# Kernel optimization log

Hardware: AMD Instinct MI355X
Metric: run time of the kernel (lower is better)

Reference implementation:

```python
import jax, jax.numpy as jnp
import numpy as np

NA = 100000   # authors
NP_ = 100000  # papers
D = 128       # hidden dim
H = 4         # heads
DH = 32       # head dim (D = H*DH)
L = 2         # layers
R = 3         # relations: 0=writes(a->p), 1=rev_writes(p->a), 2=cites(p->p)
E = 400000    # edges per relation
OUT = 40


def setup_inputs() -> dict:
    key = jax.random.key(0)
    ks = jax.random.split(key, 16)
    s = 0.05
    return {
        "x_author": jax.random.normal(ks[0], (NA, D), jnp.float32),
        "x_paper": jax.random.normal(ks[1], (NP_, D), jnp.float32),
        "ei_writes": jax.random.randint(ks[2], (2, E), 0, NA, dtype=jnp.int32),
        "ei_rev": jax.random.randint(ks[3], (2, E), 0, NA, dtype=jnp.int32),
        "ei_cites": jax.random.randint(ks[4], (2, E), 0, NP_, dtype=jnp.int32),
        "proj_w": jax.random.normal(ks[5], (2, D, D), jnp.float32) * s,
        "proj_b": jax.random.normal(ks[6], (2, D), jnp.float32) * s,
        "kqv_w": jax.random.normal(ks[7], (L, 3, 2, D, D), jnp.float32) * s,  # [layer, {k,q,v}, type, D, D]
        "kqv_b": jax.random.normal(ks[8], (L, 3, 2, D), jnp.float32) * s,
        "out_w": jax.random.normal(ks[9], (L, 2, D, D), jnp.float32) * s,
        "out_b": jax.random.normal(ks[10], (L, 2, D), jnp.float32) * s,
        "rel_a": jax.random.normal(ks[11], (L, R, H, DH, DH), jnp.float32) * s,
        "rel_m": jax.random.normal(ks[12], (L, R, H, DH, DH), jnp.float32) * s,
        "p_rel": jnp.ones((L, R, H), jnp.float32),
        "skip": jnp.ones((L, 2), jnp.float32),
        "cls_w": jax.random.normal(ks[13], (D, OUT), jnp.float32) * s,
        "cls_b": jnp.zeros((OUT,), jnp.float32),
    }


def _seg_softmax(sc, dst, n):
    # softmax over incoming edges grouped by destination node; sc: [E,H]
    m = jax.ops.segment_max(sc, dst, num_segments=n)
    m = jnp.where(jnp.isfinite(m), m, 0.0)
    e = jnp.exp(sc - m[dst])
    z = jax.ops.segment_sum(e, dst, num_segments=n)
    return e / (z[dst] + 1e-16)


def _hgt_layer(h_a, h_p, ei_w, ei_r, ei_c, kqv_w, kqv_b, out_w, out_b, rel_a, rel_m, p_rel, skip):
    na, npp = h_a.shape[0], h_p.shape[0]

    def kqv(h, t):
        k = (h @ kqv_w[0, t] + kqv_b[0, t]).reshape(-1, H, DH)
        q = (h @ kqv_w[1, t] + kqv_b[1, t]).reshape(-1, H, DH)
        v = (h @ kqv_w[2, t] + kqv_b[2, t]).reshape(-1, H, DH)
        return k, q, v

    k_a, q_a, v_a = kqv(h_a, 0)
    k_p, q_p, v_p = kqv(h_p, 1)
    scale = 1.0 / jnp.sqrt(jnp.float32(DH))

    def edge_msgs(k_src, v_src, q_dst, ei, r):
        ke = jnp.einsum('ehd,hdf->ehf', k_src[ei[0]], rel_a[r])
        ve = jnp.einsum('ehd,hdf->ehf', v_src[ei[0]], rel_m[r])
        sc = (q_dst[ei[1]] * ke).sum(-1) * p_rel[r] * scale  # [E,H]
        return sc, ve

    # destination = paper: writes (r=0) + cites (r=2); softmax jointly per dst node
    sc_w, ve_w = edge_msgs(k_a, v_a, q_p, ei_w, 0)
    sc_c, ve_c = edge_msgs(k_p, v_p, q_p, ei_c, 2)
    sc_p = jnp.concatenate([sc_w, sc_c], 0)
    ve_p = jnp.concatenate([ve_w, ve_c], 0)
    dst_p = jnp.concatenate([ei_w[1], ei_c[1]], 0)
    al_p = _seg_softmax(sc_p, dst_p, npp)
    agg_p = jax.ops.segment_sum(ve_p * al_p[..., None], dst_p, num_segments=npp).reshape(npp, D)

    # destination = author: rev_writes (r=1)
    sc_r, ve_r = edge_msgs(k_p, v_p, q_a, ei_r, 1)
    al_a = _seg_softmax(sc_r, ei_r[1], na)
    agg_a = jax.ops.segment_sum(ve_r * al_a[..., None], ei_r[1], num_segments=na).reshape(na, D)

    def out_mix(agg, h, t):
        o = jax.nn.gelu(agg, approximate=False) @ out_w[t] + out_b[t]
        s = jax.nn.sigmoid(skip[t])
        return s * o + (1.0 - s) * h

    # HGTNet.forward applies ELU after each HGTConv (dropout is identity in eval mode)
    h_a = jax.nn.elu(out_mix(agg_a, h_a, 0))
    h_p = jax.nn.elu(out_mix(agg_p, h_p, 1))
    return h_a, h_p


def reference(x_author, x_paper, ei_writes, ei_rev, ei_cites, proj_w, proj_b,
              kqv_w, kqv_b, out_w, out_b, rel_a, rel_m, p_rel, skip, cls_w, cls_b):
    h_a = x_author @ proj_w[0] + proj_b[0]
    h_p = x_paper @ proj_w[1] + proj_b[1]
    for l in range(L):
        h_a, h_p = _hgt_layer(h_a, h_p, ei_writes, ei_rev, ei_cites,
                              kqv_w[l], kqv_b[l], out_w[l], out_b[l],
                              rel_a[l], rel_m[l], p_rel[l], skip[l])
    return h_p @ cls_w + cls_b
```

## Files before the change

kernel.cpp:

```cpp
#include <hip/hip_runtime.h>
#include <hip/hip_bf16.h>
#include <math.h>

constexpr int NA  = 100000;
constexpr int NPP = 100000;
constexpr int D   = 128;
constexpr int H   = 4;
constexpr int E   = 400000;
constexpr int R   = 3;
constexpr int L   = 2;
constexpr int NSLOT = 23;
constexpr int SLOT_ELEMS = 8 * 4 * 512;
constexpr int GB2c = (NA + 127) / 128;
constexpr int GAc  = NA / 8;

using s8v = __attribute__((ext_vector_type(8))) short;
using f4v = __attribute__((ext_vector_type(4))) float;
typedef unsigned short ushort_t;

static __device__ __forceinline__ unsigned short f2bf(float f) {
  unsigned u = __float_as_uint(f);
  return (unsigned short)((u + 0x7fffu + ((u >> 16) & 1u)) >> 16);
}
static __device__ __forceinline__ float bf2f(unsigned short s) {
  return __uint_as_float(((unsigned)s) << 16);
}
static __device__ __forceinline__ float klo(int i) {
  return __uint_as_float(((unsigned)i) << 16);
}
static __device__ __forceinline__ float vhi(int i) {
  return __uint_as_float(((unsigned)i) & 0xffff0000u);
}
static __device__ __forceinline__ float gelu_f(float x) {
  return 0.5f * x * (1.0f + erff(x * 0.70710678118654752f));
}
static __device__ __forceinline__ float elu_f(float x) {
  return x > 0.0f ? x : expm1f(x);
}

static __device__ __forceinline__ void load_a2(
    const ushort_t* __restrict__ A, int ar0, int ar1, int ks, int g,
    s8v& a0, s8v& a1) {
  const ushort_t* ap0 = A + (size_t)ar0 * 128 + ks * 32 + g * 4;
  ushort4 u0 = *(const ushort4*)ap0;
  ushort4 u1 = *(const ushort4*)(ap0 + 16);
  a0[0]=(short)u0.x; a0[1]=(short)u0.y; a0[2]=(short)u0.z; a0[3]=(short)u0.w;
  a0[4]=(short)u1.x; a0[5]=(short)u1.y; a0[6]=(short)u1.z; a0[7]=(short)u1.w;
  const ushort_t* ap1 = A + (size_t)ar1 * 128 + ks * 32 + g * 4;
  ushort4 v0 = *(const ushort4*)ap1;
  ushort4 v1 = *(const ushort4*)(ap1 + 16);
  a1[0]=(short)v0.x; a1[1]=(short)v0.y; a1[2]=(short)v0.z; a1[3]=(short)v0.w;
  a1[4]=(short)v1.x; a1[5]=(short)v1.y; a1[6]=(short)v1.z; a1[7]=(short)v1.w;
}

template<bool GELU_A, bool MIX>
__device__ __forceinline__ void dev_gemm8(
    const ushort_t* __restrict__ A, const ushort_t* __restrict__ Bhi,
    const float* __restrict__ bias, ushort_t* __restrict__ Cout,
    const float* __restrict__ skip_ptr, int M, int bx, ushort_t* Bs) {
  for (int i = threadIdx.x; i < 2048; i += 256)
    *(s8v*)&Bs[i * 8] = *(const s8v*)(Bhi + (size_t)i * 8);
  __syncthreads();
  const int lane = threadIdx.x & 63;
  const int wave = threadIdx.x >> 6;
  const int row0 = bx * 128 + wave * 32;
  const int g = lane >> 4, li = lane & 15;
  f4v acc0[8], acc1[8];
#pragma unroll
  for (int ct = 0; ct < 8; ++ct) {
    acc0[ct] = f4v{0.f, 0.f, 0.f, 0.f};
    acc1[ct] = f4v{0.f, 0.f, 0.f, 0.f};
  }
  int ar0 = row0 + li;       if (ar0 >= M) ar0 = M - 1;
  int ar1 = row0 + 16 + li;  if (ar1 >= M) ar1 = M - 1;
#pragma unroll
  for (int ks = 0; ks < 4; ++ks) {
    s8v a0, a1;
    load_a2(A, ar0, ar1, ks, g, a0, a1);
    if (GELU_A) {
#pragma unroll
      for (int i = 0; i < 8; ++i) {
        a0[i] = (short)f2bf(gelu_f(bf2f((unsigned short)a0[i])));
        a1[i] = (short)f2bf(gelu_f(bf2f((unsigned short)a1[i])));
      }
    }
#pragma unroll
    for (int ct = 0; ct < 8; ++ct) {
      s8v bhi = *(const s8v*)&Bs[(ct * 4 + ks) * 512 + lane * 8];
      acc0[ct] = __builtin_amdgcn_mfma_f32_16x16x32_bf16(a0, bhi, acc0[ct], 0, 0, 0);
      acc1[ct] = __builtin_amdgcn_mfma_f32_16x16x32_bf16(a1, bhi, acc1[ct], 0, 0, 0);
    }
  }
  float sskip = 0.f;
  if (MIX) sskip = 1.f / (1.f + __expf(-*skip_ptr));
#pragma unroll
  for (int rf = 0; rf < 2; ++rf) {
#pragma unroll
    for (int ct = 0; ct < 8; ++ct) {
      int col = ct * 16 + li;
      float bv = bias[col];
      f4v a = rf ? acc1[ct] : acc0[ct];
#pragma unroll
      for (int r = 0; r < 4; ++r) {
        int grow = row0 + rf * 16 + g * 4 + r;
        if (grow < M) {
          float v = a[r] + bv;
          size_t off = (size_t)grow * 128 + col;
          if constexpr (MIX) {
            float hprev = bf2f(Cout[off]);
            Cout[off] = f2bf(elu_f(sskip * v + (1.f - sskip) * hprev));
          } else {
            Cout[off] = f2bf(v);
          }
        }
      }
    }
  }
}

__device__ __forceinline__ void dev_gemm_kv(
    const ushort_t* __restrict__ A, const ushort_t* __restrict__ Bkv,
    const float* __restrict__ bias, ushort_t* __restrict__ kvout,
    int M, int bx, int ch, ushort_t* Bs) {
  for (int i = threadIdx.x; i < 2048; i += 256) {
    int kvh = i >> 10, j = i & 1023;
    const ushort_t* src = Bkv + (size_t)kvh * SLOT_ELEMS + ch * 8192 + j * 8;
    *(s8v*)&Bs[kvh * 8192 + j * 8] = *(const s8v*)src;
  }
  __syncthreads();
  const int lane = threadIdx.x & 63;
  const int wave = threadIdx.x >> 6;
  const int row0 = bx * 128 + wave * 32;
  const int g = lane >> 4, li = lane & 15;
  f4v acc0[8], acc1[8];
#pragma unroll
  for (int t = 0; t < 8; ++t) {
    acc0[t] = f4v{0.f, 0.f, 0.f, 0.f};
    acc1[t] = f4v{0.f, 0.f, 0.f, 0.f};
  }
  int ar0 = row0 + li;       if (ar0 >= M) ar0 = M - 1;
  int ar1 = row0 + 16 + li;  if (ar1 >= M) ar1 = M - 1;
#pragma unroll
  for (int ks = 0; ks < 4; ++ks) {
    s8v a0, a1;
    load_a2(A, ar0, ar1, ks, g, a0, a1);
#pragma unroll
    for (int t = 0; t < 4; ++t) {
      s8v kh = *(const s8v*)&Bs[(t * 4 + ks) * 512 + lane * 8];
      acc0[t] = __builtin_amdgcn_mfma_f32_16x16x32_bf16(a0, kh, acc0[t], 0, 0, 0);
      acc1[t] = __builtin_amdgcn_mfma_f32_16x16x32_bf16(a1, kh, acc1[t], 0, 0, 0);
      s8v vh = *(const s8v*)&Bs[8192 + (t * 4 + ks) * 512 + lane * 8];
      acc0[4 + t] = __builtin_amdgcn_mfma_f32_16x16x32_bf16(a0, vh, acc0[4 + t], 0, 0, 0);
      acc1[4 + t] = __builtin_amdgcn_mfma_f32_16x16x32_bf16(a1, vh, acc1[4 + t], 0, 0, 0);
    }
  }
#pragma unroll
  for (int rf = 0; rf < 2; ++rf) {
#pragma unroll
    for (int t = 0; t < 4; ++t) {
      int col = ch * 64 + t * 16 + li;
      float bk = bias[col], bv = bias[128 + col];
#pragma unroll
      for (int r = 0; r < 4; ++r) {
        int grow = row0 + rf * 16 + g * 4 + r;
        if (grow < M) {
          float kvl = rf ? acc1[t][r] : acc0[t][r];
          float vvl = rf ? acc1[4 + t][r] : acc0[4 + t][r];
          ushort2 o;
          o.x = f2bf(kvl + bk);
          o.y = f2bf(vvl + bv);
          *(ushort2*)(kvout + (size_t)grow * 256 + 2 * col) = o;
        }
      }
    }
  }
}

__device__ __forceinline__ void dev_proj(
    const float* __restrict__ A, const ushort_t* __restrict__ Bhi,
    const ushort_t* __restrict__ Blo, const float* __restrict__ bias,
    ushort_t* __restrict__ Cout, int M, int bx, ushort_t* Bs) {
  for (int i = threadIdx.x; i < 4096; i += 256) {
    int half = i >> 11, j = i & 2047;
    const ushort_t* src = (half ? Blo : Bhi) + (size_t)j * 8;
    *(s8v*)&Bs[half * 16384 + j * 8] = *(const s8v*)src;
  }
  __syncthreads();
  const int lane = threadIdx.x & 63;
  const int wave = threadIdx.x >> 6;
  const int row0 = bx * 128 + wave * 32;
  const int g = lane >> 4, li = lane & 15;
  f4v acc0[8], acc1[8];
#pragma unroll
  for (int ct = 0; ct < 8; ++ct) {
    acc0[ct] = f4v{0.f, 0.f, 0.f, 0.f};
    acc1[ct] = f4v{0.f, 0.f, 0.f, 0.f};
  }
  int ar0 = row0 + li;       if (ar0 >= M) ar0 = M - 1;
  int ar1 = row0 + 16 + li;  if (ar1 >= M) ar1 = M - 1;
#pragma unroll
  for (int ks = 0; ks < 4; ++ks) {
    s8v ahi[2];
#pragma unroll
    for (int rf = 0; rf < 2; ++rf) {
      int ar = rf ? ar1 : ar0;
      const float* ap = A + (size_t)ar * 128 + ks * 32 + g * 4;
      float4 u0 = *(const float4*)ap;
      float4 u1 = *(const float4*)(ap + 16);
      float x[8] = {u0.x, u0.y, u0.z, u0.w, u1.x, u1.y, u1.z, u1.w};
#pragma unroll
      for (int i = 0; i < 8; ++i) ahi[rf][i] = (short)f2bf(x[i]);
    }
#pragma unroll
    for (int ct = 0; ct < 8; ++ct) {
      const ushort_t* bp = &Bs[(ct * 4 + ks) * 512 + lane * 8];
      s8v bhi = *(const s8v*)bp;
      s8v blo = *(const s8v*)(bp + 16384);
      acc0[ct] = __builtin_amdgcn_mfma_f32_16x16x32_bf16(ahi[0], bhi, acc0[ct], 0, 0, 0);
      acc1[ct] = __builtin_amdgcn_mfma_f32_16x16x32_bf16(ahi[1], bhi, acc1[ct], 0, 0, 0);
      acc0[ct] = __builtin_amdgcn_mfma_f32_16x16x32_bf16(ahi[0], blo, acc0[ct], 0, 0, 0);
      acc1[ct] = __builtin_amdgcn_mfma_f32_16x16x32_bf16(ahi[1], blo, acc1[ct], 0, 0, 0);
    }
  }
#pragma unroll
  for (int rf = 0; rf < 2; ++rf) {
#pragma unroll
    for (int ct = 0; ct < 8; ++ct) {
      int col = ct * 16 + li;
      float bv = bias[col];
      f4v a = rf ? acc1[ct] : acc0[ct];
#pragma unroll
      for (int r = 0; r < 4; ++r) {
        int grow = row0 + rf * 16 + g * 4 + r;
        if (grow < M) Cout[(size_t)grow * 128 + col] = f2bf(a[r] + bv);
      }
    }
  }
}

template<bool SEL>
__device__ __forceinline__ void dev_attn_m(
    const int* __restrict__ rp, const int* __restrict__ col,
    const ushort_t* __restrict__ kv, const ushort_t* __restrict__ q,
    float prW, float prC, ushort_t* __restrict__ aggout, int ablk) {
  int lane = threadIdx.x & 63;
  int wave = threadIdx.x >> 6;
  int half = lane >> 5;
  int l32  = lane & 31;
  int dst  = ablk * 8 + wave * 2 + half;
  ushort4 qv = *(const ushort4*)(q + (size_t)dst * D + l32 * 4);
  float q0 = bf2f(qv.x), q1 = bf2f(qv.y), q2 = bf2f(qv.z), q3 = bf2f(qv.w);
  int e0 = rp[dst];
  int dt = rp[dst + 1] - e0;
  float z = 0.f, a0 = 0.f, a1 = 0.f, a2 = 0.f, a3 = 0.f;
  for (int jj = 0; jj < dt; jj += 4) {
    int4 us[4]; bool vs[4]; float prs[4];
#pragma unroll
    for (int s2 = 0; s2 < 4; ++s2) {
      int idx = jj + s2;
      bool v = idx < dt;
      int ci = e0 + (v ? idx : 0);
      int row = col[ci];
      us[s2] = *(const int4*)(kv + (size_t)row * 256 + l32 * 8);
      vs[s2] = v;
      prs[s2] = SEL ? ((row >= NA) ? prC : prW) : prW;
    }
#pragma unroll
    for (int s2 = 0; s2 < 4; ++s2) {
      float p = q0 * klo(us[s2].x) + q1 * klo(us[s2].y)
              + q2 * klo(us[s2].z) + q3 * klo(us[s2].w);
      p += __shfl_xor(p, 1);
      p += __shfl_xor(p, 2);
      p += __shfl_xor(p, 4);
      float e = vs[s2] ? __expf(p * prs[s2]) : 0.f;
      z  += e;
      a0 += e * vhi(us[s2].x);
      a1 += e * vhi(us[s2].y);
      a2 += e * vhi(us[s2].z);
      a3 += e * vhi(us[s2].w);
    }
  }
  float inv = 1.f / (z + 1e-16f);
  ushort4 o;
  o.x = f2bf(a0 * inv);
  o.y = f2bf(a1 * inv);
  o.z = f2bf(a2 * inv);
  o.w = f2bf(a3 * inv);
  *(ushort4*)(aggout + (size_t)dst * D + l32 * 4) = o;
}

__device__ __forceinline__ void dev_count(const int* __restrict__ dst,
                                          int* __restrict__ deg, int bidx) {
  for (int e = bidx * 256 + (int)threadIdx.x; e < E; e += 256 * 256)
    atomicAdd(&deg[dst[e]], 1);
}
__device__ __forceinline__ void dev_fill(const int* __restrict__ ei,
                                         const int* __restrict__ rp,
                                         int* __restrict__ cnt,
                                         int* __restrict__ col, int bidx, int off) {
  const int* dst = ei + E;
  for (int e = bidx * 256 + (int)threadIdx.x; e < E; e += 256 * 256) {
    int d = dst[e];
    int pos = atomicAdd(&cnt[d], 1);
    col[rp[d] + pos] = ei[e] + off;
  }
}

__global__ __launch_bounds__(256, 2) void fusedProj(
    const float* __restrict__ x_a, const float* __restrict__ x_p,
    const ushort_t* __restrict__ B0h, const ushort_t* __restrict__ B0l,
    const ushort_t* __restrict__ B1h, const ushort_t* __restrict__ B1l,
    const float* __restrict__ proj_b,
    ushort_t* __restrict__ h_a, ushort_t* __restrict__ h_p,
    const int* __restrict__ ei_w, const int* __restrict__ ei_c,
    const int* __restrict__ ei_r, int* __restrict__ degz) {
  __shared__ ushort_t Bs[32768];
  unsigned b = blockIdx.x;
  if (b % 3 == 2) {
    int ci = b / 3;
    if (ci < 768) {
      int rel = ci >> 8, sub = ci & 255;
      const int* dst = rel == 0 ? ei_w + E : rel == 1 ? ei_c + E : ei_r + E;
      int* deg = (rel == 2) ? (degz + NPP) : degz;
      dev_count(dst, deg, sub);
    }
  } else {
    int gi = b - (b + 1) / 3;
    if (gi < GB2c) dev_proj(x_a, B0h, B0l, proj_b,     h_a, NA,  gi, Bs);
    else           dev_proj(x_p, B1h, B1l, proj_b + D, h_p, NPP, gi - GB2c, Bs);
  }
}

__device__ __forceinline__ void dev_biggemm_slice(
    int slice, int bx,
    const ushort_t* h_a, const ushort_t* h_p,
    const ushort_t* Bqa, const ushort_t* Bqp,
    const ushort_t* BkvR, const ushort_t* BkvW, const ushort_t* BkvC,
    const float* bqa, const float* bqp,
    const float* cbR, const float* cbW, const float* cbC,
    ushort_t* b_q, ushort_t* b_q2,
    ushort_t* kvR, ushort_t* kvP, ushort_t* Bs) {
  if (slice == 0)      dev_gemm8<false, false>(h_a, Bqa, bqa, b_q,  nullptr, NA,  bx, Bs);
  else if (slice == 1) dev_gemm8<false, false>(h_p, Bqp, bqp, b_q2, nullptr, NPP, bx, Bs);
  else if (slice <= 3) dev_gemm_kv(h_p, BkvR, cbR, kvR, NPP, bx, slice - 2, Bs);
  else if (slice <= 5) dev_gemm_kv(h_a, BkvW, cbW, kvP, NA,  bx, slice - 4, Bs);
  else                 dev_gemm_kv(h_p, BkvC, cbC, kvP + (size_t)NA * 256, NPP, bx, slice - 6, Bs);
}

__global__ __launch_bounds__(256, 4) void biggemm(
    const ushort_t* __restrict__ h_a, const ushort_t* __restrict__ h_p,
    const ushort_t* __restrict__ Bqa, const ushort_t* __restrict__ Bqp,
    const ushort_t* __restrict__ BkvR, const ushort_t* __restrict__ BkvW,
    const ushort_t* __restrict__ BkvC,
    const float* __restrict__ bqa, const float* __restrict__ bqp,
    const float* __restrict__ cbR, const float* __restrict__ cbW,
    const float* __restrict__ cbC,
    ushort_t* __restrict__ b_q, ushort_t* __restrict__ b_q2,
    ushort_t* __restrict__ kvR, ushort_t* __restrict__ kvP) {
  __shared__ ushort_t Bs[16384];
  dev_biggemm_slice(blockIdx.y, blockIdx.x, h_a, h_p, Bqa, Bqp, BkvR, BkvW, BkvC,
                    bqa, bqp, cbR, cbW, cbC, b_q, b_q2, kvR, kvP, Bs);
}

__global__ __launch_bounds__(256, 4) void fusedFill(
    const ushort_t* __restrict__ h_a, const ushort_t* __restrict__ h_p,
    const ushort_t* __restrict__ Bqa, const ushort_t* __restrict__ Bqp,
    const ushort_t* __restrict__ BkvR, const ushort_t* __restrict__ BkvW,
    const ushort_t* __restrict__ BkvC,
    const float* __restrict__ bqa, const float* __restrict__ bqp,
    const float* __restrict__ cbR, const float* __restrict__ cbW,
    const float* __restrict__ cbC,
    ushort_t* __restrict__ b_q, ushort_t* __restrict__ b_q2,
    ushort_t* __restrict__ kvR, ushort_t* __restrict__ kvP,
    const int* __restrict__ ei_w, const int* __restrict__ ei_c,
    const int* __restrict__ ei_r,
    const int* __restrict__ rp_p, const int* __restrict__ rp_r,
    int* __restrict__ cntz, int* __restrict__ col_p, int* __restrict__ col_r) {
  __shared__ ushort_t Bs[16384];
  unsigned b = blockIdx.x;
  if (b % 9 == 8) {
    int fi = b / 9;
    if (fi < 768) {
      int rel = fi >> 8, sub = fi & 255;
      if (rel == 0)      dev_fill(ei_w, rp_p, cntz,       col_p, sub, 0);
      else if (rel == 1) dev_fill(ei_c, rp_p, cntz,       col_p, sub, NA);
      else               dev_fill(ei_r, rp_r, cntz + NPP, col_r, sub, 0);
    }
  } else {
    int gi = b - (b + 1) / 9;
    int slice = gi & 7, bx = gi >> 3;
    if (bx < GB2c)
      dev_biggemm_slice(slice, bx, h_a, h_p, Bqa, Bqp, BkvR, BkvW, BkvC,
                        bqa, bqp, cbR, cbW, cbC, b_q, b_q2, kvR, kvP, Bs);
  }
}

__global__ __launch_bounds__(256, 8) void bigattn(
    const int* __restrict__ rp_r, const int* __restrict__ col_r,
    const ushort_t* __restrict__ kvR, ushort_t* __restrict__ q_a,
    const int* __restrict__ rp_p, const int* __restrict__ col_p,
    const ushort_t* __restrict__ kvP, ushort_t* __restrict__ q_p,
    const float* __restrict__ prelR, const float* __restrict__ prelW,
    const float* __restrict__ prelC) {
  unsigned x = blockIdx.x;
  int head = (threadIdx.x & 31) >> 3;
  const float scale = 0.17677669529663688f;
  if (x & 1) {
    float pr = prelR[head] * scale;
    dev_attn_m<false>(rp_r, col_r, kvR, q_a, pr, pr, q_a, (int)(x >> 1));
  } else {
    dev_attn_m<true>(rp_p, col_p, kvP, q_p,
                     prelW[head] * scale, prelC[head] * scale, q_p, (int)(x >> 1));
  }
}

__global__ __launch_bounds__(256, 4) void bigmix(
    const ushort_t* __restrict__ agg_a, const ushort_t* __restrict__ Bo0,
    const float* __restrict__ ob0, ushort_t* __restrict__ h_a,
    const float* __restrict__ sk0,
    const ushort_t* __restrict__ agg_p, const ushort_t* __restrict__ Bo1,
    const float* __restrict__ ob1, ushort_t* __restrict__ h_p,
    const float* __restrict__ sk1) {
  __shared__ ushort_t Bs[16384];
  if (blockIdx.y == 0) dev_gemm8<true, true>(agg_a, Bo0, ob0, h_a, sk0, NA,  blockIdx.x, Bs);
  else                 dev_gemm8<true, true>(agg_p, Bo1, ob1, h_p, sk1, NPP, blockIdx.x, Bs);
}

__global__ __launch_bounds__(256, 4) void gemm_cls(
    const ushort_t* __restrict__ A,
    const ushort_t* __restrict__ Bhi, const ushort_t* __restrict__ Blo,
    const float* __restrict__ bias, float* __restrict__ Cv, int M) {
  constexpr int NT16 = 3;
  constexpr int HN = NT16 * 2048;
  __shared__ ushort_t Bs[HN * 2];
  for (int i = threadIdx.x; i < (HN / 8) * 2; i += 256) {
    int half = i / (HN / 8), j = i % (HN / 8);
    const ushort_t* src = (half ? Blo : Bhi) + (size_t)j * 8;
    *(s8v*)&Bs[half * HN + j * 8] = *(const s8v*)src;
  }
  __syncthreads();
  const int lane = threadIdx.x & 63;
  const int wave = threadIdx.x >> 6;
  const int row0 = blockIdx.x * 128 + wave * 32;
  const int g = lane >> 4, li = lane & 15;
  f4v acc0[NT16], acc1[NT16];
#pragma unroll
  for (int ct = 0; ct < NT16; ++ct) {
    acc0[ct] = f4v{0.f, 0.f, 0.f, 0.f};
    acc1[ct] = f4v{0.f, 0.f, 0.f, 0.f};
  }
  int ar0 = row0 + li;       if (ar0 >= M) ar0 = M - 1;
  int ar1 = row0 + 16 + li;  if (ar1 >= M) ar1 = M - 1;
#pragma unroll
  for (int ks = 0; ks < 4; ++ks) {
    s8v a0, a1;
    load_a2(A, ar0, ar1, ks, g, a0, a1);
#pragma unroll
    for (int ct = 0; ct < NT16; ++ct) {
      const ushort_t* bp = &Bs[(ct * 4 + ks) * 512 + lane * 8];
      s8v bhi = *(const s8v*)bp;
      s8v blo = *(const s8v*)(bp + HN);
      acc0[ct] = __builtin_amdgcn_mfma_f32_16x16x32_bf16(a0, bhi, acc0[ct], 0, 0, 0);
      acc1[ct] = __builtin_amdgcn_mfma_f32_16x16x32_bf16(a1, bhi, acc1[ct], 0, 0, 0);
      acc0[ct] = __builtin_amdgcn_mfma_f32_16x16x32_bf16(a0, blo, acc0[ct], 0, 0, 0);
      acc1[ct] = __builtin_amdgcn_mfma_f32_16x16x32_bf16(a1, blo, acc1[ct], 0, 0, 0);
    }
  }
#pragma unroll
  for (int rf = 0; rf < 2; ++rf) {
#pragma unroll
    for (int ct = 0; ct < NT16; ++ct) {
      int col = ct * 16 + li;
      bool colok = (col < 40);
      float bv = colok ? bias[col] : 0.f;
      f4v a = rf ? acc1[ct] : acc0[ct];
#pragma unroll
      for (int r = 0; r < 4; ++r) {
        int grow = row0 + rf * 16 + g * 4 + r;
        if (grow < M && colok) Cv[(size_t)grow * 40 + col] = a[r] + bv;
      }
    }
  }
}

__global__ __launch_bounds__(256) void combine_w(
    const float* __restrict__ kqv_w, const float* __restrict__ kqv_b,
    const float* __restrict__ rel_a, const float* __restrict__ rel_m,
    float* __restrict__ cw, float* __restrict__ cb) {
  int b  = blockIdx.x;
  int kv = b & 1;
  int r  = (b >> 1) % R;
  int l  = b / (2 * R);
  int t_src = (r == 0) ? 0 : 1;
  int i_w   = (kv == 0) ? 0 : 2;
  const float* W    = kqv_w + ((size_t)((l*3 + i_w)*2 + t_src)) * D * D;
  const float* bvec = kqv_b + ((size_t)((l*3 + i_w)*2 + t_src)) * D;
  const float* rel  = ((kv == 0) ? rel_a : rel_m) + ((size_t)(l*R + r)) * H * 32 * 32;
  float* Cout = cw + (size_t)b * D * D;
  float* cbo  = cb + (size_t)b * D;
  for (int idx = threadIdx.x; idx < D * D; idx += 256) {
    int i = idx / D, j = idx % D;
    int h = j >> 5, f = j & 31;
    const float* relh = rel + h * 32 * 32;
    float sum = 0.f;
#pragma unroll
    for (int d = 0; d < 32; ++d) sum += W[i*D + (h*32 + d)] * relh[d*32 + f];
    Cout[idx] = sum;
  }
  if (threadIdx.x < D) {
    int j = threadIdx.x;
    int h = j >> 5, f = j & 31;
    const float* relh = rel + h * 32 * 32;
    float sum = 0.f;
#pragma unroll
    for (int d = 0; d < 32; ++d) sum += bvec[h*32 + d] * relh[d*32 + f];
    cbo[j] = sum;
  }
}

__global__ __launch_bounds__(256) void pack_b(
    const float* __restrict__ proj_w, const float* __restrict__ kqv_w,
    const float* __restrict__ out_w, const float* __restrict__ cls_w,
    const float* __restrict__ cw,
    ushort_t* __restrict__ phi, ushort_t* __restrict__ plo) {
  int slot = blockIdx.x;
  const float* src; int ncol = 128;
  if (slot == 0) src = proj_w;
  else if (slot == 1) src = proj_w + D * D;
  else if (slot == 22) { src = cls_w; ncol = 40; }
  else {
    int l = (slot - 2) / 10, k = (slot - 2) % 10;
    if (k == 0)      src = kqv_w + ((size_t)((l*3 + 1)*2 + 0)) * D * D;
    else if (k == 1) src = kqv_w + ((size_t)((l*3 + 1)*2 + 1)) * D * D;
    else if (k < 8)  { int idx = k - 2; src = cw + ((size_t)((l*R)*2 + idx)) * D * D; }
    else             src = out_w + ((size_t)(l*2 + (k - 8))) * D * D;
  }
  int nt = (ncol + 15) / 16;
  int total = nt * 4 * 512;
  ushort_t* ph = phi + (size_t)slot * SLOT_ELEMS;
  ushort_t* pl = plo + (size_t)slot * SLOT_ELEMS;
  for (int idx = threadIdx.x; idx < total; idx += 256) {
    int j = idx & 7, lane = (idx >> 3) & 63, ks = (idx >> 9) & 3, ct = idx >> 11;
    int k = 4 * (lane >> 4) + (j & 3) + 16 * (j >> 2) + 32 * ks;
    int n = ct * 16 + (lane & 15);
    float v = (n < ncol) ? src[(size_t)k * ncol + n] : 0.f;
    unsigned short h = f2bf(v);
    ph[idx] = h;
    pl[idx] = f2bf(v - bf2f(h));
  }
}

__global__ __launch_bounds__(256) void scan_partial(const int* __restrict__ degz,
                                                    int* __restrict__ bsum) {
  int blk = blockIdx.x, rel = blk / 25, t25 = blk % 25;
  const int* deg = degz + rel * NPP + t25 * 4096;
  int nrem = min(4096, NPP - t25 * 4096);
  int base = threadIdx.x * 16;
  int s = 0;
  if (base < nrem) {
#pragma unroll
    for (int i4 = 0; i4 < 4; ++i4) {
      int4 v = *(const int4*)(deg + base + i4 * 4);
      s += v.x + v.y + v.z + v.w;
    }
  }
  __shared__ int sm[256];
  sm[threadIdx.x] = s; __syncthreads();
  for (int o = 128; o > 0; o >>= 1) {
    if (threadIdx.x < o) sm[threadIdx.x] += sm[threadIdx.x + o];
    __syncthreads();
  }
  if (threadIdx.x == 0) bsum[blk] = sm[0];
}
__global__ __launch_bounds__(256) void scan_final(const int* __restrict__ degz,
                                                  const int* __restrict__ bsum,
                                                  int* rp_p, int* rp_r) {
  int blk = blockIdx.x, rel = blk / 25, t25 = blk % 25;
  const int* deg = degz + rel * NPP + t25 * 4096;
  int* rpb = (rel == 0 ? rp_p : rp_r);
  int* rp = rpb + t25 * 4096;
  int boffv = 0;
  for (int i = 0; i < t25; ++i) boffv += bsum[rel * 25 + i];
  int nrem = min(4096, NPP - t25 * 4096);
  int base = threadIdx.x * 16;
  bool ok = base < nrem;
  int v[16]; int s = 0;
  if (ok) {
#pragma unroll
    for (int i4 = 0; i4 < 4; ++i4) {
      int4 u = *(const int4*)(deg + base + i4 * 4);
      v[i4*4+0] = u.x; v[i4*4+1] = u.y; v[i4*4+2] = u.z; v[i4*4+3] = u.w;
      s += u.x + u.y + u.z + u.w;
    }
  }
  __shared__ int sm[256];
  sm[threadIdx.x] = s; __syncthreads();
  for (int o = 1; o < 256; o <<= 1) {
    int x = (threadIdx.x >= o) ? sm[threadIdx.x - o] : 0;
    __syncthreads(); sm[threadIdx.x] += x; __syncthreads();
  }
  int run = boffv + sm[threadIdx.x] - s;
  if (ok) {
    int w[16];
#pragma unroll
    for (int i = 0; i < 16; ++i) { w[i] = run; run += v[i]; }
#pragma unroll
    for (int i4 = 0; i4 < 4; ++i4) *(int4*)(rp + base + i4 * 4) = *(const int4*)&w[i4*4];
  }
  if (t25 == 24 && threadIdx.x == 255) rpb[NPP] = boffv + sm[255];
}

extern "C" void kernel_launch(void* const* d_in, const int* in_sizes, int n_in,
                              void* d_out, int out_size, void* d_ws, size_t ws_size,
                              hipStream_t stream) {
  const float* x_a    = (const float*)d_in[0];
  const float* x_p    = (const float*)d_in[1];
  const int*   ei_w   = (const int*)d_in[2];
  const int*   ei_r   = (const int*)d_in[3];
  const int*   ei_c   = (const int*)d_in[4];
  const float* proj_w = (const float*)d_in[5];
  const float* proj_b = (const float*)d_in[6];
  const float* kqv_w  = (const float*)d_in[7];
  const float* kqv_b  = (const float*)d_in[8];
  const float* out_w  = (const float*)d_in[9];
  const float* out_b  = (const float*)d_in[10];
  const float* rel_a  = (const float*)d_in[11];
  const float* rel_m  = (const float*)d_in[12];
  const float* p_rel  = (const float*)d_in[13];
  const float* skip   = (const float*)d_in[14];
  const float* cls_w  = (const float*)d_in[15];
  const float* cls_b  = (const float*)d_in[16];
  float* out = (float*)d_out;

  const size_t NF = (size_t)NA * D;
  char* p = (char*)d_ws;
  float* cw = (float*)p;              p += (size_t)12 * D * D * 4;
  float* cb = (float*)p;              p += (size_t)12 * D * 4;
  ushort_t* h_a   = (ushort_t*)p;     p += NF * 2;
  ushort_t* h_p   = (ushort_t*)p;     p += NF * 2;
  ushort_t* b_q   = (ushort_t*)p;     p += NF * 2;
  ushort_t* b_q2  = (ushort_t*)p;     p += NF * 2;
  ushort_t* b_kvR = (ushort_t*)p;     p += 2 * NF * 2;
  ushort_t* b_kvP = (ushort_t*)p;     p += 4 * NF * 2;
  ushort_t* phi = (ushort_t*)p;       p += (size_t)NSLOT * SLOT_ELEMS * 2;
  ushort_t* plo = (ushort_t*)p;       p += (size_t)NSLOT * SLOT_ELEMS * 2;
  int* rp_p = (int*)p;                p += (NPP + 1) * 4;
  int* rp_r = (int*)p;                p += (NA + 1) * 4;
  int* degz = (int*)p;                p += (size_t)2 * NPP * 4;
  int* cntz = (int*)p;                p += (size_t)2 * NPP * 4;
  int* col_p = (int*)p;               p += (size_t)2 * E * 4;
  int* col_r = (int*)p;               p += (size_t)E * 4;
  int* bsum = (int*)p;                p += 128 * 4;
  if (ws_size < (size_t)(p - (char*)d_ws)) return;

  hipMemsetAsync(degz, 0, sizeof(int) * 4 * (size_t)NPP, stream);

  combine_w<<<12, 256, 0, stream>>>(kqv_w, kqv_b, rel_a, rel_m, cw, cb);
  pack_b<<<NSLOT, 256, 0, stream>>>(proj_w, kqv_w, out_w, cls_w, cw, phi, plo);

  auto PH = [&](int s){ return phi + (size_t)s * SLOT_ELEMS; };
  auto PL = [&](int s){ return plo + (size_t)s * SLOT_ELEMS; };

  fusedProj<<<2346, 256, 0, stream>>>(
      x_a, x_p, PH(0), PL(0), PH(1), PL(1), proj_b, h_a, h_p,
      ei_w, ei_c, ei_r, degz);
  scan_partial<<<50, 256, 0, stream>>>(degz, bsum);
  scan_final<<<50, 256, 0, stream>>>(degz, bsum, rp_p, rp_r);

  for (int l = 0; l < L; ++l) {
    const int SQA = 2 + l * 10 + 0, SQP = 2 + l * 10 + 1;
    auto SKV = [&](int r){ return 2 + l * 10 + 2 + r * 2; };
    const int SO0 = 2 + l * 10 + 8, SO1 = 2 + l * 10 + 9;
    const float* bq_a = kqv_b + ((size_t)((l*3 + 1)*2 + 0)) * D;
    const float* bq_p = kqv_b + ((size_t)((l*3 + 1)*2 + 1)) * D;
    auto CB2 = [&](int r){ return cb + ((size_t)((l*R + r)*2)) * D; };
    const float* prelW = p_rel + (size_t)(l*R + 0) * H;
    const float* prelR = p_rel + (size_t)(l*R + 1) * H;
    const float* prelC = p_rel + (size_t)(l*R + 2) * H;

    if (l == 0) {
      fusedFill<<<7038, 256, 0, stream>>>(
          h_a, h_p, PH(SQA), PH(SQP), PH(SKV(1)), PH(SKV(0)), PH(SKV(2)),
          bq_a, bq_p, CB2(1), CB2(0), CB2(2),
          b_q, b_q2, b_kvR, b_kvP,
          ei_w, ei_c, ei_r, rp_p, rp_r, cntz, col_p, col_r);
    } else {
      biggemm<<<dim3(GB2c, 8), 256, 0, stream>>>(
          h_a, h_p, PH(SQA), PH(SQP), PH(SKV(1)), PH(SKV(0)), PH(SKV(2)),
          bq_a, bq_p, CB2(1), CB2(0), CB2(2),
          b_q, b_q2, b_kvR, b_kvP);
    }
    bigattn<<<2 * GAc, 256, 0, stream>>>(
        rp_r, col_r, b_kvR, b_q,
        rp_p, col_p, b_kvP, b_q2,
        prelR, prelW, prelC);
    bigmix<<<dim3(GB2c, 2), 256, 0, stream>>>(
        b_q,  PH(SO0), out_b + (size_t)(l*2 + 0) * D, h_a, skip + l*2 + 0,
        b_q2, PH(SO1), out_b + (size_t)(l*2 + 1) * D, h_p, skip + l*2 + 1);
  }

  gemm_cls<<<dim3(GB2c, 1), 256, 0, stream>>>(
      h_p, PH(22), PL(22), cls_b, out, NPP);
}
```

Baseline: 781.9 us.

## Drop low-half weight split in input projection and unroll paper attention deeper

The input projection GEMM no longer uses the hi/lo bf16 weight split. It loads only the high half into shared memory, which halves the MFMA count, halves LDS use, and raises launch bounds occupancy from 2 to 4. Separately, the attention gather loop is templated on its unroll factor, and paper-destination nodes (more incoming edges) now issue 8 loads in flight instead of 4. The cost is lower projection precision, since the weights are now single bf16, and higher register pressure in the attention kernel.

```diff
diff --git a/kernel.cpp b/kernel.cpp
--- a/kernel.cpp
+++ b/kernel.cpp
@@ -178,13 +178,10 @@
 
 __device__ __forceinline__ void dev_proj(
     const float* __restrict__ A, const ushort_t* __restrict__ Bhi,
-    const ushort_t* __restrict__ Blo, const float* __restrict__ bias,
-    ushort_t* __restrict__ Cout, int M, int bx, ushort_t* Bs) {
-  for (int i = threadIdx.x; i < 4096; i += 256) {
-    int half = i >> 11, j = i & 2047;
-    const ushort_t* src = (half ? Blo : Bhi) + (size_t)j * 8;
-    *(s8v*)&Bs[half * 16384 + j * 8] = *(const s8v*)src;
-  }
+    const float* __restrict__ bias, ushort_t* __restrict__ Cout,
+    int M, int bx, ushort_t* Bs) {
+  for (int i = threadIdx.x; i < 2048; i += 256)
+    *(s8v*)&Bs[i * 8] = *(const s8v*)(Bhi + (size_t)i * 8);
   __syncthreads();
   const int lane = threadIdx.x & 63;
   const int wave = threadIdx.x >> 6;
@@ -213,13 +210,9 @@
     }
 #pragma unroll
     for (int ct = 0; ct < 8; ++ct) {
-      const ushort_t* bp = &Bs[(ct * 4 + ks) * 512 + lane * 8];
-      s8v bhi = *(const s8v*)bp;
-      s8v blo = *(const s8v*)(bp + 16384);
+      s8v bhi = *(const s8v*)&Bs[(ct * 4 + ks) * 512 + lane * 8];
       acc0[ct] = __builtin_amdgcn_mfma_f32_16x16x32_bf16(ahi[0], bhi, acc0[ct], 0, 0, 0);
       acc1[ct] = __builtin_amdgcn_mfma_f32_16x16x32_bf16(ahi[1], bhi, acc1[ct], 0, 0, 0);
-      acc0[ct] = __builtin_amdgcn_mfma_f32_16x16x32_bf16(ahi[0], blo, acc0[ct], 0, 0, 0);
-      acc1[ct] = __builtin_amdgcn_mfma_f32_16x16x32_bf16(ahi[1], blo, acc1[ct], 0, 0, 0);
     }
   }
 #pragma unroll
@@ -238,7 +231,7 @@
   }
 }
 
-template<bool SEL>
+template<bool SEL, int UN>
 __device__ __forceinline__ void dev_attn_m(
     const int* __restrict__ rp, const int* __restrict__ col,
     const ushort_t* __restrict__ kv, const ushort_t* __restrict__ q,
@@ -253,10 +246,10 @@
   int e0 = rp[dst];
   int dt = rp[dst + 1] - e0;
   float z = 0.f, a0 = 0.f, a1 = 0.f, a2 = 0.f, a3 = 0.f;
-  for (int jj = 0; jj < dt; jj += 4) {
-    int4 us[4]; bool vs[4]; float prs[4];
-#pragma unroll
-    for (int s2 = 0; s2 < 4; ++s2) {
+  for (int jj = 0; jj < dt; jj += UN) {
+    int4 us[UN]; bool vs[UN]; float prs[UN];
+#pragma unroll
+    for (int s2 = 0; s2 < UN; ++s2) {
       int idx = jj + s2;
       bool v = idx < dt;
       int ci = e0 + (v ? idx : 0);
@@ -266,7 +259,7 @@
       prs[s2] = SEL ? ((row >= NA) ? prC : prW) : prW;
     }
 #pragma unroll
-    for (int s2 = 0; s2 < 4; ++s2) {
+    for (int s2 = 0; s2 < UN; ++s2) {
       float p = q0 * klo(us[s2].x) + q1 * klo(us[s2].y)
               + q2 * klo(us[s2].z) + q3 * klo(us[s2].w);
       p += __shfl_xor(p, 1);
@@ -306,15 +299,14 @@
   }
 }
 
-__global__ __launch_bounds__(256, 2) void fusedProj(
+__global__ __launch_bounds__(256, 4) void fusedProj(
     const float* __restrict__ x_a, const float* __restrict__ x_p,
-    const ushort_t* __restrict__ B0h, const ushort_t* __restrict__ B0l,
-    const ushort_t* __restrict__ B1h, const ushort_t* __restrict__ B1l,
+    const ushort_t* __restrict__ B0h, const ushort_t* __restrict__ B1h,
     const float* __restrict__ proj_b,
     ushort_t* __restrict__ h_a, ushort_t* __restrict__ h_p,
     const int* __restrict__ ei_w, const int* __restrict__ ei_c,
     const int* __restrict__ ei_r, int* __restrict__ degz) {
-  __shared__ ushort_t Bs[32768];
+  __shared__ ushort_t Bs[16384];
   unsigned b = blockIdx.x;
   if (b % 3 == 2) {
     int ci = b / 3;
@@ -326,8 +318,8 @@
     }
   } else {
     int gi = b - (b + 1) / 3;
-    if (gi < GB2c) dev_proj(x_a, B0h, B0l, proj_b,     h_a, NA,  gi, Bs);
-    else           dev_proj(x_p, B1h, B1l, proj_b + D, h_p, NPP, gi - GB2c, Bs);
+    if (gi < GB2c) dev_proj(x_a, B0h, proj_b,     h_a, NA,  gi, Bs);
+    else           dev_proj(x_p, B1h, proj_b + D, h_p, NPP, gi - GB2c, Bs);
   }
 }
 
@@ -407,10 +399,10 @@
   const float scale = 0.17677669529663688f;
   if (x & 1) {
     float pr = prelR[head] * scale;
-    dev_attn_m<false>(rp_r, col_r, kvR, q_a, pr, pr, q_a, (int)(x >> 1));
+    dev_attn_m<false, 4>(rp_r, col_r, kvR, q_a, pr, pr, q_a, (int)(x >> 1));
   } else {
-    dev_attn_m<true>(rp_p, col_p, kvP, q_p,
-                     prelW[head] * scale, prelC[head] * scale, q_p, (int)(x >> 1));
+    dev_attn_m<true, 8>(rp_p, col_p, kvP, q_p,
+                        prelW[head] * scale, prelC[head] * scale, q_p, (int)(x >> 1));
   }
 }
 
@@ -662,7 +654,7 @@
   auto PL = [&](int s){ return plo + (size_t)s * SLOT_ELEMS; };
 
   fusedProj<<<2346, 256, 0, stream>>>(
-      x_a, x_p, PH(0), PL(0), PH(1), PL(1), proj_b, h_a, h_p,
+      x_a, x_p, PH(0), PH(1), proj_b, h_a, h_p,
       ei_w, ei_c, ei_r, degz);
   scan_partial<<<50, 256, 0, stream>>>(degz, bsum);
   scan_final<<<50, 256, 0, stream>>>(degz, bsum, rp_p, rp_r);
```

Result: slower. 984.4 us (+25.9%).
